# Performance work log

Measured on AMD Instinct MI355X. Metric: run time of the kernel, lower is better.

Reference implementation:

```python
import jax, jax.numpy as jnp
import numpy as np

K = 9                 # kernel_size (num_points)
CENTER = K // 2
EXTEND_SCOPE = 1.0
EPS = 1e-5
GROUPS = 4            # out_ch // 4


def _cumsum_from_center(o):
    # o: [N, K, D, W, H]; serial offset accumulation outward from center row,
    # vectorized as two cumsums (matches the torch for-loop recurrence).
    upper = jnp.cumsum(o[:, CENTER:], axis=1)                                   # rows c..K-1
    lower = jnp.flip(jnp.cumsum(jnp.flip(o[:, :CENTER + 1], axis=1), axis=1), axis=1)  # rows 0..c
    return jnp.concatenate([lower[:, :CENTER], upper], axis=1)


def _coordinate_map_3d(offset):
    # offset: [N, 3K, D, W, H] -> (z, y, x) coord maps, each [N, D, W, H*K]  (morph=0, if_offset=True)
    N, _, D, W, H = offset.shape
    dt = offset.dtype
    z_off, y_off, _x_off = jnp.split(offset, 3, axis=1)   # each [N, K, D, W, H]
    z_acc = _cumsum_from_center(z_off)
    y_acc = _cumsum_from_center(y_off)
    z_c = jnp.arange(D, dtype=dt)[None, None, :, None, None]
    y_c = jnp.arange(W, dtype=dt)[None, None, None, :, None]
    x_c = jnp.arange(H, dtype=dt)[None, None, None, None, :]
    x_g = (jnp.arange(K, dtype=dt) - CENTER)[None, :, None, None, None]  # linspace(-c, c, K)
    z_new = z_c + EXTEND_SCOPE * z_acc                 # [N, K, D, W, H]
    y_new = y_c + EXTEND_SCOPE * y_acc
    x_new = jnp.broadcast_to(x_c + x_g, z_new.shape)

    def pack(a):  # [N,K,D,W,H] -> [N,D,W,H*K] (permute(0,4,1,5,2,6,3) + reshape in torch)
        return jnp.transpose(a, (0, 2, 3, 4, 1)).reshape(N, D, W, H * K)

    return pack(z_new), pack(y_new), pack(x_new)


def _trilinear_interpolate(feat, z, y, x):
    # feat: [N, C, D, W, H]; z/y/x: [N, D, W, HK] -> [N, C, D, W, HK]
    N, C, D, W, H = feat.shape
    featp = jnp.transpose(feat, (0, 2, 3, 4, 1))  # [N, D, W, H, C]
    z0 = jnp.clip(jnp.floor(z).astype(jnp.int32), 0, D - 1)
    z1 = jnp.clip(jnp.floor(z).astype(jnp.int32) + 1, 0, D - 1)
    y0 = jnp.clip(jnp.floor(y).astype(jnp.int32), 0, W - 1)
    y1 = jnp.clip(jnp.floor(y).astype(jnp.int32) + 1, 0, W - 1)
    x0 = jnp.clip(jnp.floor(x).astype(jnp.int32), 0, H - 1)
    x1 = jnp.clip(jnp.floor(x).astype(jnp.int32) + 1, 0, H - 1)
    z0f, z1f = z0.astype(feat.dtype), z1.astype(feat.dtype)
    y0f, y1f = y0.astype(feat.dtype), y1.astype(feat.dtype)
    x0f, x1f = x0.astype(feat.dtype), x1.astype(feat.dtype)
    b = jnp.arange(N)[:, None, None, None]

    def g(zi, yi, xi):
        return featp[b, zi, yi, xi]  # gather -> [N, D, W, HK, C]

    out = (g(z0, y0, x0) * ((z1f - z) * (y1f - y) * (x1f - x))[..., None]
         + g(z0, y0, x1) * ((z1f - z) * (y1f - y) * (x - x0f))[..., None]
         + g(z0, y1, x0) * ((z1f - z) * (y - y0f) * (x1f - x))[..., None]
         + g(z0, y1, x1) * ((z1f - z) * (y - y0f) * (x - x0f))[..., None]
         + g(z1, y0, x0) * ((z - z0f) * (y1f - y) * (x1f - x))[..., None]
         + g(z1, y0, x1) * ((z - z0f) * (y1f - y) * (x - x0f))[..., None]
         + g(z1, y1, x0) * ((z - z0f) * (y - y0f) * (x1f - x))[..., None]
         + g(z1, y1, x1) * ((z - z0f) * (y - y0f) * (x - x0f))[..., None])
    return jnp.transpose(out, (0, 4, 1, 2, 3))  # [N, C, D, W, HK]


def _conv3d(x, w, b, stride, padding):
    out = jax.lax.conv_general_dilated(x, w, window_strides=stride, padding=padding,
                                       dimension_numbers=('NCDHW', 'OIDHW', 'NCDHW'))
    return out + b[None, :, None, None, None]


def _batchnorm(x, gamma, beta):
    mu = jnp.mean(x, axis=(0, 2, 3, 4), keepdims=True)
    var = jnp.var(x, axis=(0, 2, 3, 4), keepdims=True)
    xn = (x - mu) * jax.lax.rsqrt(var + EPS)
    return gamma[None, :, None, None, None] * xn + beta[None, :, None, None, None]


def _groupnorm(x, gamma, beta):
    N, C = x.shape[:2]
    xg = x.reshape(N, GROUPS, C // GROUPS, *x.shape[2:])
    mu = jnp.mean(xg, axis=(2, 3, 4, 5), keepdims=True)
    var = jnp.var(xg, axis=(2, 3, 4, 5), keepdims=True)
    xn = ((xg - mu) * jax.lax.rsqrt(var + EPS)).reshape(x.shape)
    return gamma[None, :, None, None, None] * xn + beta[None, :, None, None, None]


def setup_inputs() -> dict:
    key = jax.random.key(0)
    ks = jax.random.split(key, 5)
    N, Cin, Cout, D, W, H = 1, 8, 16, 64, 64, 64
    f = jax.random.normal(ks[0], (N, Cin, D, W, H), dtype=jnp.float32)
    off_w = jax.random.normal(ks[1], (3 * K, Cin, 3, 3, 3), dtype=jnp.float32) * 0.05
    off_b = jax.random.normal(ks[2], (3 * K,), dtype=jnp.float32) * 0.05
    bn_g = jnp.ones((3 * K,), jnp.float32)
    bn_b = jnp.zeros((3 * K,), jnp.float32)
    dcn_w = jax.random.normal(ks[3], (Cout, Cin, 1, 1, K), dtype=jnp.float32) * 0.1
    dcn_b = jax.random.normal(ks[4], (Cout,), dtype=jnp.float32) * 0.05
    gn_g = jnp.ones((Cout,), jnp.float32)
    gn_b = jnp.zeros((Cout,), jnp.float32)
    return {"f": f, "off_w": off_w, "off_b": off_b, "bn_g": bn_g, "bn_b": bn_b,
            "dcn_w": dcn_w, "dcn_b": dcn_b, "gn_g": gn_g, "gn_b": gn_b}


def reference(f, off_w, off_b, bn_g, bn_b, dcn_w, dcn_b, gn_g, gn_b):
    # offset branch: Conv3d(in, 3K, 3, pad 1) -> BN -> tanh
    offset = _conv3d(f, off_w, off_b, (1, 1, 1), [(1, 1), (1, 1), (1, 1)])
    offset = jnp.tanh(_batchnorm(offset, bn_g, bn_b))
    # deformable coordinate map (morph=0) + trilinear gather
    z, y, x = _coordinate_map_3d(offset)
    deformed = _trilinear_interpolate(f, z, y, x)        # [N, C, D, W, H*K]
    # fused conv along the extended axis: kernel (1,1,K), stride (1,1,K)
    out = _conv3d(deformed, dcn_w, dcn_b, (1, 1, K), [(0, 0), (0, 0), (0, 0)])
    return jax.nn.relu(_groupnorm(out, gn_g, gn_b))      # [N, out, D, W, H]
```

## Files before the change

kernel.cpp:

```cpp
#include <hip/hip_runtime.h>
#include <math.h>

#define VOX 262144

__device__ __forceinline__ int clampi(int v, int lo, int hi) {
    return v < lo ? lo : (v > hi ? hi : v);
}

__global__ void k_pre(const float* __restrict__ f, float* __restrict__ ft,
                      const float* __restrict__ w, float* __restrict__ wT,
                      float* __restrict__ stats) {
    int vox = blockIdx.x * 256 + threadIdx.x;
    float v[8];
#pragma unroll
    for (int ci = 0; ci < 8; ci++) v[ci] = f[ci * VOX + vox];
    float4* dst = (float4*)(ft + (size_t)vox * 8);
    dst[0] = make_float4(v[0], v[1], v[2], v[3]);
    dst[1] = make_float4(v[4], v[5], v[6], v[7]);

    if (blockIdx.x == 0) {
        if (threadIdx.x < 64) stats[threadIdx.x] = 0.f;
    } else if (blockIdx.x == 1) {
        for (int i = threadIdx.x; i < 3888; i += 256) {
            int c = i / 216, r = i % 216;
            int ci = r / 27, k = r % 27;
            wT[(k * 8 + ci) * 18 + c] = w[i];
        }
    }
}

__global__ __launch_bounds__(256) void k_conv_off(
        const float* __restrict__ f, const float* __restrict__ wT,
        const float* __restrict__ b, float* __restrict__ offs,
        float* __restrict__ stats) {
    __shared__ float tile[8 * 3 * 6 * 64];
    int tid = threadIdx.x;
    int blk = blockIdx.x;
    int d = blk >> 4;
    int wy0 = (blk & 15) << 2;

#pragma unroll
    for (int j = 0; j < 9; j++) {
        int flat = j * 256 + tid;
        int row = flat >> 4;
        int off = (flat & 15) << 2;
        int ci = row / 18, rem = row % 18;
        int kd = rem / 6, wl = rem % 6;
        int dd = clampi(d + kd - 1, 0, 63);
        int ww = clampi(wy0 + wl - 1, 0, 63);
        *(float4*)(tile + row * 64 + off) =
            *(const float4*)(f + ci * VOX + (dd * 64 + ww) * 64 + off);
    }
    __syncthreads();

    int h = tid & 63, wl0 = tid >> 6;
    int wy = wy0 + wl0;
    int idx = blk * 256 + tid;

    int hc0 = h > 0 ? h - 1 : 0;
    int hc2 = h < 63 ? h + 1 : 63;
    float mh0 = h > 0 ? 1.f : 0.f;
    float mh2 = h < 63 ? 1.f : 0.f;

    float acc[18];
#pragma unroll
    for (int c = 0; c < 18; c++) acc[c] = b[c];

#pragma unroll
    for (int s = 0; s < 9; s++) {
        int kd = s / 3, kw = s % 3;
        int dd = d + kd - 1, ww = wy + kw - 1;
        bool ok = ((unsigned)dd < 64u) & ((unsigned)ww < 64u);
        if (ok) {
            const float* wrow = wT + s * 432;
#pragma unroll
            for (int ci = 0; ci < 8; ci++) {
                const float* lp = tile + (ci * 18 + kd * 6 + wl0 + kw) * 64;
                float v0 = lp[hc0] * mh0;
                float v1 = lp[h];
                float v2 = lp[hc2] * mh2;
                const float* wp = wrow + ci * 18;
#pragma unroll
                for (int c = 0; c < 18; c++) {
                    float a = acc[c];
                    a = fmaf(v0, wp[c], a);
                    a = fmaf(v1, wp[144 + c], a);
                    a = fmaf(v2, wp[288 + c], a);
                    acc[c] = a;
                }
            }
        }
    }

#pragma unroll
    for (int c = 0; c < 18; c++) offs[c * VOX + idx] = acc[c];

    __shared__ float ls[36];
    if (tid < 36) ls[tid] = 0.f;
    __syncthreads();
#pragma unroll
    for (int c = 0; c < 18; c++) {
        float s = acc[c], q = acc[c] * acc[c];
#pragma unroll
        for (int o = 32; o > 0; o >>= 1) {
            s += __shfl_xor(s, o);
            q += __shfl_xor(q, o);
        }
        if ((tid & 63) == 0) {
            atomicAdd(&ls[c], s);
            atomicAdd(&ls[18 + c], q);
        }
    }
    __syncthreads();
    if (tid < 36) atomicAdd(&stats[tid], ls[tid]);
}

__global__ __launch_bounds__(256) void k_main(
        const float* __restrict__ ft, const float* __restrict__ offs,
        const float* __restrict__ stats, const float* __restrict__ bn_g,
        const float* __restrict__ bn_b, const float* __restrict__ dw,
        const float* __restrict__ db, float* __restrict__ out,
        float* __restrict__ gstats) {
    int idx = blockIdx.x * 256 + threadIdx.x;
    int h = idx & 63, wy = (idx >> 6) & 63, d = idx >> 12;
    const float inv = 1.f / (float)VOX;

    float zo[9], yo[9];
#pragma unroll
    for (int c = 0; c < 18; c++) {
        float m = stats[c] * inv;
        float var = stats[18 + c] * inv - m * m;
        float rs = rsqrtf(var + 1e-5f);
        float t = tanhf(bn_g[c] * ((offs[c * VOX + idx] - m) * rs) + bn_b[c]);
        if (c < 9) zo[c] = t; else yo[c - 9] = t;
    }

    float za[9], ya[9];
    za[4] = zo[4]; ya[4] = yo[4];
#pragma unroll
    for (int k = 5; k < 9; k++) { za[k] = za[k - 1] + zo[k]; ya[k] = ya[k - 1] + yo[k]; }
#pragma unroll
    for (int k = 3; k >= 0; k--) { za[k] = za[k + 1] + zo[k]; ya[k] = ya[k + 1] + yo[k]; }

    float acc[16];
#pragma unroll
    for (int co = 0; co < 16; co++) acc[co] = db[co];

#pragma unroll
    for (int k = 0; k < 9; k++) {
        int xi = h + k - 4;
        if (xi >= 0 && xi <= 62) {
            float z = (float)d + za[k];
            float y = (float)wy + ya[k];
            float fz = floorf(z), fy = floorf(y);
            int iz = (int)fz, iy = (int)fy;
            int z0 = clampi(iz, 0, 63), z1 = clampi(iz + 1, 0, 63);
            int y0 = clampi(iy, 0, 63), y1 = clampi(iy + 1, 0, 63);
            float wz0 = (float)z1 - z, wz1 = z - (float)z0;
            float wy0 = (float)y1 - y, wy1 = y - (float)y0;
            float w00 = wz0 * wy0, w01 = wz0 * wy1, w10 = wz1 * wy0, w11 = wz1 * wy1;

            const float4* p00 = (const float4*)(ft + (((z0 * 64 + y0) * 64 + xi) << 3));
            const float4* p01 = (const float4*)(ft + (((z0 * 64 + y1) * 64 + xi) << 3));
            const float4* p10 = (const float4*)(ft + (((z1 * 64 + y0) * 64 + xi) << 3));
            const float4* p11 = (const float4*)(ft + (((z1 * 64 + y1) * 64 + xi) << 3));
            float4 a00 = p00[0], b00 = p00[1];
            float4 a01 = p01[0], b01 = p01[1];
            float4 a10 = p10[0], b10 = p10[1];
            float4 a11 = p11[0], b11 = p11[1];

            float v[8];
            v[0] = w00 * a00.x + w01 * a01.x + w10 * a10.x + w11 * a11.x;
            v[1] = w00 * a00.y + w01 * a01.y + w10 * a10.y + w11 * a11.y;
            v[2] = w00 * a00.z + w01 * a01.z + w10 * a10.z + w11 * a11.z;
            v[3] = w00 * a00.w + w01 * a01.w + w10 * a10.w + w11 * a11.w;
            v[4] = w00 * b00.x + w01 * b01.x + w10 * b10.x + w11 * b11.x;
            v[5] = w00 * b00.y + w01 * b01.y + w10 * b10.y + w11 * b11.y;
            v[6] = w00 * b00.z + w01 * b01.z + w10 * b10.z + w11 * b11.z;
            v[7] = w00 * b00.w + w01 * b01.w + w10 * b10.w + w11 * b11.w;

#pragma unroll
            for (int ci = 0; ci < 8; ci++) {
#pragma unroll
                for (int co = 0; co < 16; co++)
                    acc[co] = fmaf(v[ci], dw[(co * 8 + ci) * 9 + k], acc[co]);
            }
        }
    }

#pragma unroll
    for (int co = 0; co < 16; co++) out[co * VOX + idx] = acc[co];

    __shared__ float ls[8];
    if (threadIdx.x < 8) ls[threadIdx.x] = 0.f;
    __syncthreads();
#pragma unroll
    for (int g = 0; g < 4; g++) {
        float s = acc[4 * g] + acc[4 * g + 1] + acc[4 * g + 2] + acc[4 * g + 3];
        float q = acc[4 * g] * acc[4 * g] + acc[4 * g + 1] * acc[4 * g + 1]
                + acc[4 * g + 2] * acc[4 * g + 2] + acc[4 * g + 3] * acc[4 * g + 3];
#pragma unroll
        for (int o = 32; o > 0; o >>= 1) {
            s += __shfl_xor(s, o);
            q += __shfl_xor(q, o);
        }
        if ((threadIdx.x & 63) == 0) {
            atomicAdd(&ls[g], s);
            atomicAdd(&ls[4 + g], q);
        }
    }
    __syncthreads();
    if (threadIdx.x < 8) atomicAdd(&gstats[threadIdx.x], ls[threadIdx.x]);
}

__global__ void k_gn(const float* __restrict__ gstats, const float* __restrict__ gn_g,
                     const float* __restrict__ gn_b, float* __restrict__ out) {
    int i = blockIdx.x * 256 + threadIdx.x;
    int c = i >> 16;
    int g = c >> 2;
    const float invn = 1.f / (4.f * (float)VOX);
    float m = gstats[g] * invn;
    float var = gstats[4 + g] * invn - m * m;
    float rs = rsqrtf(var + 1e-5f);
    float gg = gn_g[c], gb = gn_b[c];
    float4 v = ((float4*)out)[i];
    v.x = (v.x - m) * rs * gg + gb; v.x = v.x > 0.f ? v.x : 0.f;
    v.y = (v.y - m) * rs * gg + gb; v.y = v.y > 0.f ? v.y : 0.f;
    v.z = (v.z - m) * rs * gg + gb; v.z = v.z > 0.f ? v.z : 0.f;
    v.w = (v.w - m) * rs * gg + gb; v.w = v.w > 0.f ? v.w : 0.f;
    ((float4*)out)[i] = v;
}

extern "C" void kernel_launch(void* const* d_in, const int* in_sizes, int n_in,
                              void* d_out, int out_size, void* d_ws, size_t ws_size,
                              hipStream_t stream) {
    const float* f    = (const float*)d_in[0];
    const float* offw = (const float*)d_in[1];
    const float* offb = (const float*)d_in[2];
    const float* bng  = (const float*)d_in[3];
    const float* bnb  = (const float*)d_in[4];
    const float* dcnw = (const float*)d_in[5];
    const float* dcnb = (const float*)d_in[6];
    const float* gng  = (const float*)d_in[7];
    const float* gnb  = (const float*)d_in[8];
    float* out = (float*)d_out;

    float* ws    = (float*)d_ws;
    float* ft    = ws;
    float* offs  = ws + 8 * VOX;
    float* stats = offs + 18 * VOX;
    float* gstats = stats + 36;
    float* wT = out;

    hipLaunchKernelGGL(k_pre, dim3(VOX / 256), dim3(256), 0, stream, f, ft, offw, wT, stats);
    hipLaunchKernelGGL(k_conv_off, dim3(VOX / 256), dim3(256), 0, stream,
                       f, wT, offb, offs, stats);
    hipLaunchKernelGGL(k_main, dim3(VOX / 256), dim3(256), 0, stream,
                       ft, offs, stats, bng, bnb, dcnw, dcnb, out, gstats);
    hipLaunchKernelGGL(k_gn, dim3((16 * VOX / 4) / 256), dim3(256), 0, stream,
                       gstats, gng, gnb, out);
}
```

Measured before the change: 188.5 us.

## Fuse input transpose and weight transpose into offset conv kernel

Removes the separate pre-pass kernel by writing the channel-last copy of the input from the shared-memory tile already loaded in the offset conv kernel. The conv now reads the original weight layout directly instead of a pre-transposed copy, and the stats buffer is zeroed with a memset. This saves one full read of the input and one kernel launch. The strided weight reads (stride 216 per output channel) may be less cache-friendly than the contiguous transposed layout, though they are uniform across threads.

```diff
diff --git a/kernel.cpp b/kernel.cpp
--- a/kernel.cpp
+++ b/kernel.cpp
@@ -7,32 +7,10 @@
     return v < lo ? lo : (v > hi ? hi : v);
 }
 
-__global__ void k_pre(const float* __restrict__ f, float* __restrict__ ft,
-                      const float* __restrict__ w, float* __restrict__ wT,
-                      float* __restrict__ stats) {
-    int vox = blockIdx.x * 256 + threadIdx.x;
-    float v[8];
-#pragma unroll
-    for (int ci = 0; ci < 8; ci++) v[ci] = f[ci * VOX + vox];
-    float4* dst = (float4*)(ft + (size_t)vox * 8);
-    dst[0] = make_float4(v[0], v[1], v[2], v[3]);
-    dst[1] = make_float4(v[4], v[5], v[6], v[7]);
-
-    if (blockIdx.x == 0) {
-        if (threadIdx.x < 64) stats[threadIdx.x] = 0.f;
-    } else if (blockIdx.x == 1) {
-        for (int i = threadIdx.x; i < 3888; i += 256) {
-            int c = i / 216, r = i % 216;
-            int ci = r / 27, k = r % 27;
-            wT[(k * 8 + ci) * 18 + c] = w[i];
-        }
-    }
-}
-
-__global__ __launch_bounds__(256) void k_conv_off(
-        const float* __restrict__ f, const float* __restrict__ wT,
-        const float* __restrict__ b, float* __restrict__ offs,
-        float* __restrict__ stats) {
+__global__ __launch_bounds__(256) void k_front(
+        const float* __restrict__ f, const float* __restrict__ offw,
+        const float* __restrict__ offb, float* __restrict__ ft,
+        float* __restrict__ offs, float* __restrict__ stats) {
     __shared__ float tile[8 * 3 * 6 * 64];
     int tid = threadIdx.x;
     int blk = blockIdx.x;
@@ -57,6 +35,15 @@
     int wy = wy0 + wl0;
     int idx = blk * 256 + tid;
 
+    {
+        float v[8];
+#pragma unroll
+        for (int ci = 0; ci < 8; ci++) v[ci] = tile[(ci * 18 + 6 + wl0 + 1) * 64 + h];
+        float4* dst = (float4*)(ft + (size_t)idx * 8);
+        dst[0] = make_float4(v[0], v[1], v[2], v[3]);
+        dst[1] = make_float4(v[4], v[5], v[6], v[7]);
+    }
+
     int hc0 = h > 0 ? h - 1 : 0;
     int hc2 = h < 63 ? h + 1 : 63;
     float mh0 = h > 0 ? 1.f : 0.f;
@@ -64,7 +51,7 @@
 
     float acc[18];
 #pragma unroll
-    for (int c = 0; c < 18; c++) acc[c] = b[c];
+    for (int c = 0; c < 18; c++) acc[c] = offb[c];
 
 #pragma unroll
     for (int s = 0; s < 9; s++) {
@@ -72,20 +59,19 @@
         int dd = d + kd - 1, ww = wy + kw - 1;
         bool ok = ((unsigned)dd < 64u) & ((unsigned)ww < 64u);
         if (ok) {
-            const float* wrow = wT + s * 432;
 #pragma unroll
             for (int ci = 0; ci < 8; ci++) {
                 const float* lp = tile + (ci * 18 + kd * 6 + wl0 + kw) * 64;
                 float v0 = lp[hc0] * mh0;
                 float v1 = lp[h];
                 float v2 = lp[hc2] * mh2;
-                const float* wp = wrow + ci * 18;
+                const float* wp = offw + ci * 27 + s * 3;
 #pragma unroll
                 for (int c = 0; c < 18; c++) {
                     float a = acc[c];
-                    a = fmaf(v0, wp[c], a);
-                    a = fmaf(v1, wp[144 + c], a);
-                    a = fmaf(v2, wp[288 + c], a);
+                    a = fmaf(v0, wp[c * 216 + 0], a);
+                    a = fmaf(v1, wp[c * 216 + 1], a);
+                    a = fmaf(v2, wp[c * 216 + 2], a);
                     acc[c] = a;
                 }
             }
@@ -245,18 +231,16 @@
     const float* gnb  = (const float*)d_in[8];
     float* out = (float*)d_out;
 
-    float* ws    = (float*)d_ws;
-    float* ft    = ws;
-    float* offs  = ws + 8 * VOX;
-    float* stats = offs + 18 * VOX;
-    float* gstats = stats + 36;
-    float* wT = out;
-
-    hipLaunchKernelGGL(k_pre, dim3(VOX / 256), dim3(256), 0, stream, f, ft, offw, wT, stats);
-    hipLaunchKernelGGL(k_conv_off, dim3(VOX / 256), dim3(256), 0, stream,
-                       f, wT, offb, offs, stats);
+    float* ws     = (float*)d_ws;
+    float* ft     = ws;
+    float* offs   = ws + 8 * VOX;
+    float* stats  = offs + 18 * VOX;
+
+    hipMemsetAsync(stats, 0, 44 * sizeof(float), stream);
+    hipLaunchKernelGGL(k_front, dim3(VOX / 256), dim3(256), 0, stream,
+                       f, offw, offb, ft, offs, stats);
     hipLaunchKernelGGL(k_main, dim3(VOX / 256), dim3(256), 0, stream,
-                       ft, offs, stats, bng, bnb, dcnw, dcnb, out, gstats);
+                       ft, offs, stats, bng, bnb, dcnw, dcnb, out, stats + 36);
     hipLaunchKernelGGL(k_gn, dim3((16 * VOX / 4) / 256), dim3(256), 0, stream,
-                       gstats, gng, gnb, out);
-}
+                       stats + 36, gng, gnb, out);
+}
```

After: 203.1 us. +7.7%, slower.
